# Optimization experiments

Measured on AMD Instinct MI355X. Metric: run time of the kernel, lower is better.

The kernel has to match this reference:

```python
import jax, jax.numpy as jnp
import numpy as np

N_NODES = 50000
N_EDGES = 800000
N_IN = 96
N_HID = 96
N_CLS = 16
P_DROP = 0.5


def setup_inputs() -> dict:
    key = jax.random.key(0)
    ks = jax.random.split(key, 10)
    return {
        "features": jax.random.normal(ks[0], (N_NODES, N_IN), dtype=jnp.float32),
        "edge_weight": jax.random.uniform(ks[1], (N_EDGES,), dtype=jnp.float32),
        "src": jax.random.randint(ks[2], (N_EDGES,), 0, N_NODES),
        "dst": jax.random.randint(ks[3], (N_EDGES,), 0, N_NODES),
        "W0": jax.random.normal(ks[4], (N_IN, N_HID), dtype=jnp.float32) / np.sqrt(N_IN).astype(np.float32),
        "b0": jnp.zeros((N_HID,), dtype=jnp.float32),
        "W1": jax.random.normal(ks[5], (N_HID, N_HID), dtype=jnp.float32) / np.sqrt(N_HID).astype(np.float32),
        "b1": jnp.zeros((N_HID,), dtype=jnp.float32),
        "W2": jax.random.normal(ks[6], (N_HID, N_CLS), dtype=jnp.float32) / np.sqrt(N_HID).astype(np.float32),
        "b2": jnp.zeros((N_CLS,), dtype=jnp.float32),
    }


def reference(features, edge_weight, src, dst, W0, b0, W1, b1, W2, b2):
    N = features.shape[0]
    # Unweighted node degrees (DGL GraphConv norm='both'), clamped to >= 1.
    ones_e = jnp.ones_like(edge_weight)
    out_deg = jnp.clip(jax.ops.segment_sum(ones_e, src, num_segments=N), 1.0)
    in_deg = jnp.clip(jax.ops.segment_sum(ones_e, dst, num_segments=N), 1.0)
    inv_sqrt_out = out_deg ** -0.5  # [N]
    inv_sqrt_in = in_deg ** -0.5    # [N]

    def graph_conv(h, W, b, act):
        h = h * inv_sqrt_out[:, None]
        m = h[src] * edge_weight[:, None]                   # [E, d] gather + edge scale
        agg = jax.ops.segment_sum(m, dst, num_segments=N)   # [N, d] scatter-add
        out = (agg * inv_sqrt_in[:, None]) @ W + b          # D_in^-1/2, then linear + bias
        return act(out) if act is not None else out

    layers = [(W0, b0, jax.nn.relu), (W1, b1, jax.nn.relu), (W2, b2, None)]
    dkey = jax.random.key(42)
    h = features
    for i, (W, b, act) in enumerate(layers):
        keep = jax.random.bernoulli(jax.random.fold_in(dkey, i), 1.0 - P_DROP, h.shape)
        h = jnp.where(keep, h / (1.0 - P_DROP), 0.0)        # dropout p=0.5
        h = graph_conv(h, W, b, act)
    return jax.nn.log_softmax(h, axis=1)
```

## Files before the change

kernel.cpp:

```cpp
#include <hip/hip_runtime.h>
#include <hip/hip_fp16.h>
#include <stdint.h>

#define NNODES 50000
#define NEDGES 800000
#define NHID 96
#define NCLS 16
#define NB ((NNODES + 255) / 256)

#define NC 200
#define NR 4
#define EPB (NEDGES / NC)
#define RNODES (NNODES / NR)
#define RWORDS8 (RNODES / 4)
#define NWORDS8 (NNODES / 4)
#define NDROP4 ((NNODES * NHID / 4 + 255) / 256)

__host__ __device__ inline void tf2x32(uint32_t k0, uint32_t k1, uint32_t x0, uint32_t x1,
                                       uint32_t& o0, uint32_t& o1) {
  uint32_t k2 = k0 ^ k1 ^ 0x1BD11BDAu;
#define TFROT(v, r) (((v) << (r)) | ((v) >> (32 - (r))))
#define TFR(r) { x0 += x1; x1 = TFROT(x1, r); x1 ^= x0; }
  x0 += k0; x1 += k1;
  TFR(13) TFR(15) TFR(26) TFR(6)
  x0 += k1; x1 += k2 + 1u;
  TFR(17) TFR(29) TFR(16) TFR(24)
  x0 += k2; x1 += k0 + 2u;
  TFR(13) TFR(15) TFR(26) TFR(6)
  x0 += k0; x1 += k1 + 3u;
  TFR(17) TFR(29) TFR(16) TFR(24)
  x0 += k1; x1 += k2 + 4u;
  TFR(13) TFR(15) TFR(26) TFR(6)
  x0 += k2; x1 += k0 + 5u;
  o0 = x0; o1 = x1;
#undef TFR
#undef TFROT
}

__device__ inline bool keep_bit(uint32_t k0, uint32_t k1, uint32_t j) {
  uint32_t o0, o1;
  tf2x32(k0, k1, 0u, j, o0, o1);
  return (((o0 ^ o1) >> 31) == 0u);
}

__global__ __launch_bounds__(256) void hist_kernel(
    const int* __restrict__ src, const int* __restrict__ dst,
    uint32_t* __restrict__ slabD, uint32_t* __restrict__ slabS) {
  __shared__ uint32_t HD[RWORDS8];
  __shared__ uint32_t HS[RWORDS8];
  const int tid = threadIdx.x, b = blockIdx.x;
  const int c = b / NR, r = b - c * NR;
  const int e0 = c * EPB, e1 = e0 + EPB;
  const int nbase = r * RNODES;
  for (int w = tid; w < RWORDS8; w += 256) { HD[w] = 0; HS[w] = 0; }
  __syncthreads();
  int e = e0 + tid;
  for (; e + 768 < e1; e += 1024) {
    int d0 = dst[e] - nbase,       d1 = dst[e + 256] - nbase;
    int d2 = dst[e + 512] - nbase, d3 = dst[e + 768] - nbase;
    int s0 = src[e] - nbase,       s1 = src[e + 256] - nbase;
    int s2 = src[e + 512] - nbase, s3 = src[e + 768] - nbase;
    if ((unsigned)d0 < (unsigned)RNODES) atomicAdd(&HD[d0 >> 2], 1u << ((d0 & 3) * 8));
    if ((unsigned)d1 < (unsigned)RNODES) atomicAdd(&HD[d1 >> 2], 1u << ((d1 & 3) * 8));
    if ((unsigned)d2 < (unsigned)RNODES) atomicAdd(&HD[d2 >> 2], 1u << ((d2 & 3) * 8));
    if ((unsigned)d3 < (unsigned)RNODES) atomicAdd(&HD[d3 >> 2], 1u << ((d3 & 3) * 8));
    if ((unsigned)s0 < (unsigned)RNODES) atomicAdd(&HS[s0 >> 2], 1u << ((s0 & 3) * 8));
    if ((unsigned)s1 < (unsigned)RNODES) atomicAdd(&HS[s1 >> 2], 1u << ((s1 & 3) * 8));
    if ((unsigned)s2 < (unsigned)RNODES) atomicAdd(&HS[s2 >> 2], 1u << ((s2 & 3) * 8));
    if ((unsigned)s3 < (unsigned)RNODES) atomicAdd(&HS[s3 >> 2], 1u << ((s3 & 3) * 8));
  }
  for (; e < e1; e += 256) {
    int d = dst[e] - nbase;
    if ((unsigned)d < (unsigned)RNODES) atomicAdd(&HD[d >> 2], 1u << ((d & 3) * 8));
    int s = src[e] - nbase;
    if ((unsigned)s < (unsigned)RNODES) atomicAdd(&HS[s >> 2], 1u << ((s & 3) * 8));
  }
  __syncthreads();
  uint32_t* dpD = slabD + (size_t)b * RWORDS8;
  uint32_t* dpS = slabS + (size_t)b * RWORDS8;
  for (int w = tid; w < RWORDS8; w += 256) { dpD[w] = HD[w]; dpS[w] = HS[w]; }
}

__global__ __launch_bounds__(256) void reduce_base_kernel(
    const uint32_t* __restrict__ slabD, const uint32_t* __restrict__ slabS,
    int* __restrict__ ideg, float* __restrict__ inv_o, float* __restrict__ inv_i,
    uint32_t* __restrict__ rel8) {
  int gw = blockIdx.x * 256 + threadIdx.x;
  if (gw >= NWORDS8) return;
  int r = gw / RWORDS8, lw = gw - r * RWORDS8;
  int n0 = r * RNODES + 4 * lw;
  uint32_t runD = 0, runS = 0;
#pragma unroll 4
  for (int c = 0; c < NC; ++c) {
    rel8[(size_t)c * NWORDS8 + gw] = runD;
    runD += slabD[(size_t)(c * NR + r) * RWORDS8 + lw];
    runS += slabS[(size_t)(c * NR + r) * RWORDS8 + lw];
  }
  int d0 = runD & 0xFF, d1 = (runD >> 8) & 0xFF, d2 = (runD >> 16) & 0xFF, d3 = runD >> 24;
  int o0 = runS & 0xFF, o1 = (runS >> 8) & 0xFF, o2 = (runS >> 16) & 0xFF, o3 = runS >> 24;
  *(int4*)(ideg + n0) = make_int4(d0, d1, d2, d3);
  *(float4*)(inv_i + n0) = make_float4(
      rsqrtf(fmaxf((float)d0, 1.0f)), rsqrtf(fmaxf((float)d1, 1.0f)),
      rsqrtf(fmaxf((float)d2, 1.0f)), rsqrtf(fmaxf((float)d3, 1.0f)));
  *(float4*)(inv_o + n0) = make_float4(
      rsqrtf(fmaxf((float)o0, 1.0f)), rsqrtf(fmaxf((float)o1, 1.0f)),
      rsqrtf(fmaxf((float)o2, 1.0f)), rsqrtf(fmaxf((float)o3, 1.0f)));
}

__global__ __launch_bounds__(256) void scan_blocks_kernel(
    const int* __restrict__ ideg, int* __restrict__ bsum) {
  __shared__ int lds[256];
  const int tid = threadIdx.x;
  int i = blockIdx.x * 256 + tid;
  lds[tid] = (i < NNODES) ? ideg[i] : 0;
  __syncthreads();
  for (int off = 128; off > 0; off >>= 1) {
    if (tid < off) lds[tid] += lds[tid + off];
    __syncthreads();
  }
  if (tid == 0) bsum[blockIdx.x] = lds[0];
}

__global__ __launch_bounds__(256) void scan_top_kernel(
    const int* __restrict__ bsum, int* __restrict__ boff) {
  __shared__ int lds[256];
  const int tid = threadIdx.x;
  int v = (tid < NB) ? bsum[tid] : 0;
  lds[tid] = v;
  __syncthreads();
  for (int off = 1; off < 256; off <<= 1) {
    int t = (tid >= off) ? lds[tid - off] : 0;
    __syncthreads();
    lds[tid] += t;
    __syncthreads();
  }
  if (tid < NB) boff[tid] = lds[tid] - v;
}

__global__ __launch_bounds__(256) void scan_write_kernel(
    const int* __restrict__ ideg, const int* __restrict__ boff,
    int* __restrict__ row_ptr) {
  __shared__ int lds[256];
  const int tid = threadIdx.x;
  int i = blockIdx.x * 256 + tid;
  int v = (i < NNODES) ? ideg[i] : 0;
  lds[tid] = v;
  __syncthreads();
  for (int off = 1; off < 256; off <<= 1) {
    int t = (tid >= off) ? lds[tid - off] : 0;
    __syncthreads();
    lds[tid] += t;
    __syncthreads();
  }
  if (i < NNODES) row_ptr[i] = boff[blockIdx.x] + lds[tid] - v;
  if (i == 0) row_ptr[NNODES] = NEDGES;
}

__global__ __launch_bounds__(256) void fill_drop_kernel(
    const int* __restrict__ src, const int* __restrict__ dst, const float* __restrict__ ew,
    const uint32_t* __restrict__ rel8, const int* __restrict__ row_ptr,
    uint32_t* __restrict__ csr,
    const float* __restrict__ h, const float* __restrict__ inv_o,
    float* __restrict__ X, uint32_t k0, uint32_t k1) {
  __shared__ uint32_t H[RWORDS8];
  const int tid = threadIdx.x, b = blockIdx.x;
  if (b >= NC * NR) {
    int j = ((b - NC * NR) * 256 + tid) * 4;
    if (j < NNODES * NHID) {
      int n = j / NHID;
      float4 hv = *(const float4*)(h + j);
      float sc = 2.0f * inv_o[n];
      float4 o;
      o.x = keep_bit(k0, k1, (uint32_t)(j + 0)) ? hv.x * sc : 0.0f;
      o.y = keep_bit(k0, k1, (uint32_t)(j + 1)) ? hv.y * sc : 0.0f;
      o.z = keep_bit(k0, k1, (uint32_t)(j + 2)) ? hv.z * sc : 0.0f;
      o.w = keep_bit(k0, k1, (uint32_t)(j + 3)) ? hv.w * sc : 0.0f;
      *(float4*)(X + j) = o;
    }
    return;
  }
  const int c = b / NR, r = b - c * NR;
  const int e0 = c * EPB, e1 = e0 + EPB;
  const int nbase = r * RNODES;
  const uint32_t* rel = rel8 + (size_t)c * NWORDS8;
  for (int w = tid; w < RWORDS8; w += 256) H[w] = 0;
  __syncthreads();
  int e = e0 + tid;
  for (; e + 256 < e1; e += 512) {
    int da = dst[e], db = dst[e + 256];
    int sa = src[e], sb = src[e + 256];
    float wa = ew[e], wb = ew[e + 256];
    int la = da - nbase, lb = db - nbase;
    bool ia = (unsigned)la < (unsigned)RNODES;
    bool ib = (unsigned)lb < (unsigned)RNODES;
    if (ia) {
      int sh = (la & 3) * 8;
      uint32_t old = atomicAdd(&H[la >> 2], 1u << sh);
      int rank = (int)((old >> sh) & 0xFFu);
      int rel_v = (int)((rel[da >> 2] >> ((da & 3) * 8)) & 0xFFu);
      int pos = row_ptr[da] + rel_v + rank;
      if ((unsigned)pos < (unsigned)NEDGES) {
        uint32_t v = ((uint32_t)sa << 16) | (uint32_t)__half_as_ushort(__float2half_rn(wa));
        __builtin_nontemporal_store(v, &csr[pos]);
      }
    }
    if (ib) {
      int sh = (lb & 3) * 8;
      uint32_t old = atomicAdd(&H[lb >> 2], 1u << sh);
      int rank = (int)((old >> sh) & 0xFFu);
      int rel_v = (int)((rel[db >> 2] >> ((db & 3) * 8)) & 0xFFu);
      int pos = row_ptr[db] + rel_v + rank;
      if ((unsigned)pos < (unsigned)NEDGES) {
        uint32_t v = ((uint32_t)sb << 16) | (uint32_t)__half_as_ushort(__float2half_rn(wb));
        __builtin_nontemporal_store(v, &csr[pos]);
      }
    }
  }
  for (; e < e1; e += 256) {
    int d = dst[e];
    int ld = d - nbase;
    if ((unsigned)ld < (unsigned)RNODES) {
      int sh = (ld & 3) * 8;
      uint32_t old = atomicAdd(&H[ld >> 2], 1u << sh);
      int rank = (int)((old >> sh) & 0xFFu);
      int rel_v = (int)((rel[d >> 2] >> ((d & 3) * 8)) & 0xFFu);
      int pos = row_ptr[d] + rel_v + rank;
      if ((unsigned)pos < (unsigned)NEDGES) {
        uint32_t v = ((uint32_t)src[e] << 16) | (uint32_t)__half_as_ushort(__float2half_rn(ew[e]));
        __builtin_nontemporal_store(v, &csr[pos]);
      }
    }
  }
}

__global__ __launch_bounds__(256) void gemm96_kernel(
    const float* __restrict__ X, const float* __restrict__ W, __half* __restrict__ Yh) {
  __shared__ float Wl[96 * 96];
  const int tid = threadIdx.x;
  {
    const float4* Wg = (const float4*)W;
    float4* Ws = (float4*)Wl;
#pragma unroll
    for (int i = 0; i < 9; ++i)
      Ws[tid + i * 256] = Wg[tid + i * 256];
  }
  __syncthreads();

  const int cg = tid & 7;
  const int rq = tid >> 3;
  const int row0 = blockIdx.x * 128 + rq * 4;
  const int c0 = cg * 12;

  float acc[4][12];
#pragma unroll
  for (int r = 0; r < 4; ++r)
#pragma unroll
    for (int c = 0; c < 12; ++c) acc[r][c] = 0.f;

  const float* xr[4];
#pragma unroll
  for (int r = 0; r < 4; ++r) {
    int rr = row0 + r; if (rr > NNODES - 1) rr = NNODES - 1;
    xr[r] = X + (size_t)rr * 96;
  }

  for (int k = 0; k < 96; k += 4) {
    float4 x4[4];
#pragma unroll
    for (int r = 0; r < 4; ++r) x4[r] = *(const float4*)(xr[r] + k);
#pragma unroll
    for (int kk = 0; kk < 4; ++kk) {
      const float4* wp = (const float4*)(Wl + (k + kk) * 96 + c0);
      float4 w0 = wp[0], w1 = wp[1], w2 = wp[2];
      float xv[4] = { (&x4[0].x)[kk], (&x4[1].x)[kk], (&x4[2].x)[kk], (&x4[3].x)[kk] };
#pragma unroll
      for (int r = 0; r < 4; ++r) {
        acc[r][0]  += xv[r] * w0.x; acc[r][1]  += xv[r] * w0.y;
        acc[r][2]  += xv[r] * w0.z; acc[r][3]  += xv[r] * w0.w;
        acc[r][4]  += xv[r] * w1.x; acc[r][5]  += xv[r] * w1.y;
        acc[r][6]  += xv[r] * w1.z; acc[r][7]  += xv[r] * w1.w;
        acc[r][8]  += xv[r] * w2.x; acc[r][9]  += xv[r] * w2.y;
        acc[r][10] += xv[r] * w2.z; acc[r][11] += xv[r] * w2.w;
      }
    }
  }

#pragma unroll
  for (int r = 0; r < 4; ++r) {
    int rr = row0 + r;
    if (rr < NNODES) {
      __half2* hp = (__half2*)(Yh + (size_t)rr * 96 + c0);
#pragma unroll
      for (int c = 0; c < 6; ++c)
        hp[c] = __floats2half2_rn(acc[r][2 * c], acc[r][2 * c + 1]);
    }
  }
}

__global__ __launch_bounds__(256) void gemm16_kernel(
    const float* __restrict__ X, const float* __restrict__ W, __half* __restrict__ Y2h) {
  __shared__ float Wl[96 * 16];
  const int tid = threadIdx.x;
  {
    const float4* Wg = (const float4*)W;
    float4* Ws = (float4*)Wl;
    for (int i = tid; i < 384; i += 256) Ws[i] = Wg[i];
  }
  __syncthreads();

  const int row0 = blockIdx.x * 512 + tid * 2;
  const float* xr[2];
#pragma unroll
  for (int r = 0; r < 2; ++r) {
    int rr = row0 + r; if (rr > NNODES - 1) rr = NNODES - 1;
    xr[r] = X + (size_t)rr * 96;
  }

  float acc[2][16];
#pragma unroll
  for (int r = 0; r < 2; ++r)
#pragma unroll
    for (int c = 0; c < 16; ++c) acc[r][c] = 0.f;

  for (int k = 0; k < 96; k += 4) {
    float4 x4[2];
#pragma unroll
    for (int r = 0; r < 2; ++r) x4[r] = *(const float4*)(xr[r] + k);
#pragma unroll
    for (int kk = 0; kk < 4; ++kk) {
      const float4* wp = (const float4*)(Wl + (k + kk) * 16);
      float4 w0 = wp[0], w1 = wp[1], w2 = wp[2], w3 = wp[3];
#pragma unroll
      for (int r = 0; r < 2; ++r) {
        float xv = (&x4[r].x)[kk];
        acc[r][0]  += xv * w0.x; acc[r][1]  += xv * w0.y;
        acc[r][2]  += xv * w0.z; acc[r][3]  += xv * w0.w;
        acc[r][4]  += xv * w1.x; acc[r][5]  += xv * w1.y;
        acc[r][6]  += xv * w1.z; acc[r][7]  += xv * w1.w;
        acc[r][8]  += xv * w2.x; acc[r][9]  += xv * w2.y;
        acc[r][10] += xv * w2.z; acc[r][11] += xv * w2.w;
        acc[r][12] += xv * w3.x; acc[r][13] += xv * w3.y;
        acc[r][14] += xv * w3.z; acc[r][15] += xv * w3.w;
      }
    }
  }

#pragma unroll
  for (int r = 0; r < 2; ++r) {
    int rr = row0 + r;
    if (rr < NNODES) {
      __half2* hp = (__half2*)(Y2h + (size_t)rr * 16);
#pragma unroll
      for (int c = 0; c < 8; ++c)
        hp[c] = __floats2half2_rn(acc[r][2 * c], acc[r][2 * c + 1]);
    }
  }
}

#define ACC16(u0, u1, wt) { \
  float2 g0 = __half22float2(*(__half2*)&u0.x); \
  float2 g1 = __half22float2(*(__half2*)&u0.y); \
  float2 g2 = __half22float2(*(__half2*)&u0.z); \
  float2 g3 = __half22float2(*(__half2*)&u0.w); \
  float2 g4 = __half22float2(*(__half2*)&u1.x); \
  float2 g5 = __half22float2(*(__half2*)&u1.y); \
  float2 g6 = __half22float2(*(__half2*)&u1.z); \
  float2 g7 = __half22float2(*(__half2*)&u1.w); \
  acc[0]  += g0.x * wt; acc[1]  += g0.y * wt; \
  acc[2]  += g1.x * wt; acc[3]  += g1.y * wt; \
  acc[4]  += g2.x * wt; acc[5]  += g2.y * wt; \
  acc[6]  += g3.x * wt; acc[7]  += g3.y * wt; \
  acc[8]  += g4.x * wt; acc[9]  += g4.y * wt; \
  acc[10] += g5.x * wt; acc[11] += g5.y * wt; \
  acc[12] += g6.x * wt; acc[13] += g6.y * wt; \
  acc[14] += g7.x * wt; acc[15] += g7.y * wt; }

__global__ __launch_bounds__(256) void gather96_drop_kernel(
    const __half* __restrict__ Yh, const uint32_t* __restrict__ csr,
    const int* __restrict__ row_ptr, const float* __restrict__ inv_in,
    const float* __restrict__ inv_o, const float* __restrict__ bias,
    float* __restrict__ Xn, uint32_t k0, uint32_t k1) {
  int tid = blockIdx.x * 256 + threadIdx.x;
  int n = tid / 6;
  int q = tid - n * 6;
  if (n >= NNODES) return;
  int beg = row_ptr[n], end = row_ptr[n + 1];
  float acc[16];
#pragma unroll
  for (int i = 0; i < 16; ++i) acc[i] = 0.f;

  int p = beg;
  for (; p + 4 <= end; p += 4) {
    uint32_t pa = csr[p], pb = csr[p + 1], pc = csr[p + 2], pd = csr[p + 3];
    int s0 = pa >> 16, s1 = pb >> 16, s2 = pc >> 16, s3 = pd >> 16;
    if (s0 >= NNODES) s0 = 0;
    if (s1 >= NNODES) s1 = 0;
    if (s2 >= NNODES) s2 = 0;
    if (s3 >= NNODES) s3 = 0;
    float w0 = __half2float(__ushort_as_half((unsigned short)(pa & 0xFFFFu)));
    float w1 = __half2float(__ushort_as_half((unsigned short)(pb & 0xFFFFu)));
    float w2 = __half2float(__ushort_as_half((unsigned short)(pc & 0xFFFFu)));
    float w3 = __half2float(__ushort_as_half((unsigned short)(pd & 0xFFFFu)));
    const uint4* y0 = (const uint4*)(Yh + (size_t)s0 * 96 + q * 16);
    const uint4* y1 = (const uint4*)(Yh + (size_t)s1 * 96 + q * 16);
    const uint4* y2 = (const uint4*)(Yh + (size_t)s2 * 96 + q * 16);
    const uint4* y3 = (const uint4*)(Yh + (size_t)s3 * 96 + q * 16);
    uint4 a0 = y0[0], a1 = y0[1];
    uint4 b0 = y1[0], b1 = y1[1];
    uint4 c0 = y2[0], c1 = y2[1];
    uint4 d0 = y3[0], d1 = y3[1];
    ACC16(a0, a1, w0)
    ACC16(b0, b1, w1)
    ACC16(c0, c1, w2)
    ACC16(d0, d1, w3)
  }
  for (; p + 2 <= end; p += 2) {
    uint32_t pa = csr[p], pb = csr[p + 1];
    int s0 = pa >> 16, s1 = pb >> 16;
    if (s0 >= NNODES) s0 = 0;
    if (s1 >= NNODES) s1 = 0;
    float w0 = __half2float(__ushort_as_half((unsigned short)(pa & 0xFFFFu)));
    float w1 = __half2float(__ushort_as_half((unsigned short)(pb & 0xFFFFu)));
    const uint4* y0 = (const uint4*)(Yh + (size_t)s0 * 96 + q * 16);
    const uint4* y1 = (const uint4*)(Yh + (size_t)s1 * 96 + q * 16);
    uint4 a0 = y0[0], a1 = y0[1];
    uint4 b0 = y1[0], b1 = y1[1];
    ACC16(a0, a1, w0)
    ACC16(b0, b1, w1)
  }
  if (p < end) {
    uint32_t pa = csr[p];
    int s0 = pa >> 16;
    if (s0 >= NNODES) s0 = 0;
    float w0 = __half2float(__ushort_as_half((unsigned short)(pa & 0xFFFFu)));
    const uint4* y0 = (const uint4*)(Yh + (size_t)s0 * 96 + q * 16);
    uint4 a0 = y0[0], a1 = y0[1];
    ACC16(a0, a1, w0)
  }

  float iv = inv_in[n];
  float sc = 2.0f * inv_o[n];
  const float* bp = bias + q * 16;
  float o[16];
#pragma unroll
  for (int i = 0; i < 16; ++i)
    o[i] = fmaxf(acc[i] * iv + bp[i], 0.f) * sc;
  uint32_t jb = (uint32_t)(n * 96 + q * 16);
#pragma unroll
  for (int i = 0; i < 16; ++i)
    o[i] = keep_bit(k0, k1, jb + i) ? o[i] : 0.f;
  float* xp = Xn + (size_t)n * 96 + q * 16;
  *(float4*)(xp + 0)  = make_float4(o[0], o[1], o[2], o[3]);
  *(float4*)(xp + 4)  = make_float4(o[4], o[5], o[6], o[7]);
  *(float4*)(xp + 8)  = make_float4(o[8], o[9], o[10], o[11]);
  *(float4*)(xp + 12) = make_float4(o[12], o[13], o[14], o[15]);
}

__global__ __launch_bounds__(256) void gather16_lsm_kernel(
    const __half* __restrict__ Y2h, const uint32_t* __restrict__ csr,
    const int* __restrict__ row_ptr, const float* __restrict__ inv_in,
    const float* __restrict__ b2, float* __restrict__ out) {
  int n = blockIdx.x * 256 + threadIdx.x;
  if (n >= NNODES) return;
  int beg = row_ptr[n], end = row_ptr[n + 1];
  float acc[16];
#pragma unroll
  for (int i = 0; i < 16; ++i) acc[i] = 0.f;

  int p = beg;
  for (; p + 2 <= end; p += 2) {
    uint32_t pa = csr[p], pb = csr[p + 1];
    int sa = pa >> 16, sb = pb >> 16;
    if (sa >= NNODES) sa = 0;
    if (sb >= NNODES) sb = 0;
    float wa = __half2float(__ushort_as_half((unsigned short)(pa & 0xFFFFu)));
    float wb = __half2float(__ushort_as_half((unsigned short)(pb & 0xFFFFu)));
    const uint4* ya = (const uint4*)(Y2h + (size_t)sa * 16);
    const uint4* yb = (const uint4*)(Y2h + (size_t)sb * 16);
    uint4 a0 = ya[0], a1 = ya[1];
    uint4 b0 = yb[0], b1 = yb[1];
    ACC16(a0, a1, wa)
    ACC16(b0, b1, wb)
  }
  if (p < end) {
    uint32_t pa = csr[p];
    int sa = pa >> 16;
    if (sa >= NNODES) sa = 0;
    float wa = __half2float(__ushort_as_half((unsigned short)(pa & 0xFFFFu)));
    const uint4* ya = (const uint4*)(Y2h + (size_t)sa * 16);
    uint4 a0 = ya[0], a1 = ya[1];
    ACC16(a0, a1, wa)
  }

  float iv = inv_in[n];
  float v[16];
#pragma unroll
  for (int i = 0; i < 16; ++i) v[i] = acc[i] * iv + b2[i];
  float m = v[0];
#pragma unroll
  for (int i = 1; i < 16; i++) m = fmaxf(m, v[i]);
  float s = 0.f;
#pragma unroll
  for (int i = 0; i < 16; i++) s += expf(v[i] - m);
  float ls = logf(s);
  float* orow = out + (size_t)n * 16;
#pragma unroll
  for (int i = 0; i < 16; i++) orow[i] = v[i] - m - ls;
}

extern "C" void kernel_launch(void* const* d_in, const int* in_sizes, int n_in,
                              void* d_out, int out_size, void* d_ws, size_t ws_size,
                              hipStream_t stream) {
  const float* feat = (const float*)d_in[0];
  const float* ew   = (const float*)d_in[1];
  const int*   src  = (const int*)d_in[2];
  const int*   dst  = (const int*)d_in[3];
  const float* W0   = (const float*)d_in[4];
  const float* b0   = (const float*)d_in[5];
  const float* W1   = (const float*)d_in[6];
  const float* b1   = (const float*)d_in[7];
  const float* W2   = (const float*)d_in[8];
  const float* b2   = (const float*)d_in[9];
  float* out = (float*)d_out;

  char* base = (char*)d_ws;
  size_t off = 0;
  auto take = [&](size_t nbytes) {
    void* q = base + off;
    off += (nbytes + 255) & ~(size_t)255;
    return q;
  };
  int*      ideg    = (int*)take((size_t)NNODES * 4);
  int*      row_ptr = (int*)take((size_t)(NNODES + 1) * 4);
  int*      bsum    = (int*)take((size_t)NB * 4);
  int*      boff    = (int*)take((size_t)NB * 4);
  float*    inv_o   = (float*)take((size_t)NNODES * 4);
  float*    inv_i   = (float*)take((size_t)NNODES * 4);
  uint32_t* slabD   = (uint32_t*)take((size_t)NC * NR * RWORDS8 * 4);
  uint32_t* slabS   = (uint32_t*)take((size_t)NC * NR * RWORDS8 * 4);
  uint32_t* rel8    = (uint32_t*)take((size_t)NC * NWORDS8 * 4);
  uint32_t* csr     = (uint32_t*)take((size_t)NEDGES * 4);
  float*    X       = (float*)take((size_t)NNODES * NHID * 4);
  __half*   Yh      = (__half*)take((size_t)NNODES * NHID * 2);
  __half*   Y2h     = (__half*)take((size_t)NNODES * NCLS * 2);
  (void)ws_size; (void)in_sizes; (void)n_in; (void)out_size;

  uint32_t k[3][2];
  for (uint32_t i = 0; i < 3; i++) tf2x32(0u, 42u, 0u, i, k[i][0], k[i][1]);

  const int GW = (NWORDS8 + 255) / 256;

  hist_kernel<<<NC * NR, 256, 0, stream>>>(src, dst, slabD, slabS);
  reduce_base_kernel<<<GW, 256, 0, stream>>>(slabD, slabS, ideg, inv_o, inv_i, rel8);
  scan_blocks_kernel<<<NB, 256, 0, stream>>>(ideg, bsum);
  scan_top_kernel<<<1, 256, 0, stream>>>(bsum, boff);
  scan_write_kernel<<<NB, 256, 0, stream>>>(ideg, boff, row_ptr);
  fill_drop_kernel<<<NC * NR + NDROP4, 256, 0, stream>>>(
      src, dst, ew, rel8, row_ptr, csr, feat, inv_o, X, k[0][0], k[0][1]);

  const int G96  = (NNODES + 127) / 128;
  const int G16  = (NNODES + 511) / 512;
  const int GGD  = (NNODES * 6 + 255) / 256;

  gemm96_kernel<<<G96, 256, 0, stream>>>(X, W0, Yh);
  gather96_drop_kernel<<<GGD, 256, 0, stream>>>(Yh, csr, row_ptr, inv_i, inv_o, b0, X, k[1][0], k[1][1]);
  gemm96_kernel<<<G96, 256, 0, stream>>>(X, W1, Yh);
  gather96_drop_kernel<<<GGD, 256, 0, stream>>>(Yh, csr, row_ptr, inv_i, inv_o, b1, X, k[2][0], k[2][1]);
  gemm16_kernel<<<G16, 256, 0, stream>>>(X, W2, Y2h);
  gather16_lsm_kernel<<<(NNODES + 255) / 256, 256, 0, stream>>>(Y2h, csr, row_ptr, inv_i, b2, out);
}
```

Measured before the change: 292.5 us.

## Fuse degree reduce with decoupled-lookback scan, halve chunk count, widen gather

Merges the reduce, block-scan, top-scan and scan-write kernels into one reduce_scan kernel. It computes row_ptr with a single-pass scan where each block publishes its sum through flags and later blocks spin-wait on earlier ones, removing three launches and the ideg/bsum round trips. The edge chunk count NC drops from 200 to 100, which halves the slab and rel8 traffic but makes each histogram block longer. gather96 now uses 3 threads per node with 32 features each instead of 6 threads with 16, trading more registers and less parallelism for fewer redundant CSR reads. The spin-wait assumes earlier blocks are scheduled first, which holds here with only 49 blocks but is not guaranteed in general.

```diff
diff --git a/kernel.cpp b/kernel.cpp
--- a/kernel.cpp
+++ b/kernel.cpp
@@ -6,14 +6,15 @@
 #define NEDGES 800000
 #define NHID 96
 #define NCLS 16
-#define NB ((NNODES + 255) / 256)
-
-#define NC 200
+
+#define NC 100
 #define NR 4
 #define EPB (NEDGES / NC)
 #define RNODES (NNODES / NR)
 #define RWORDS8 (RNODES / 4)
 #define NWORDS8 (NNODES / 4)
+#define SCANB ((NWORDS8 + 255) / 256)
+#define FILLBLKS (NC * NR)
 #define NDROP4 ((NNODES * NHID / 4 + 255) / 256)
 
 __host__ __device__ inline void tf2x32(uint32_t k0, uint32_t k1, uint32_t x0, uint32_t x1,
@@ -45,10 +46,12 @@
 
 __global__ __launch_bounds__(256) void hist_kernel(
     const int* __restrict__ src, const int* __restrict__ dst,
-    uint32_t* __restrict__ slabD, uint32_t* __restrict__ slabS) {
+    uint32_t* __restrict__ slabD, uint32_t* __restrict__ slabS,
+    uint32_t* __restrict__ flags) {
   __shared__ uint32_t HD[RWORDS8];
   __shared__ uint32_t HS[RWORDS8];
   const int tid = threadIdx.x, b = blockIdx.x;
+  if (b == 0 && tid < SCANB) flags[tid] = 0;
   const int c = b / NR, r = b - c * NR;
   const int e0 = c * EPB, e1 = e0 + EPB;
   const int nbase = r * RNODES;
@@ -81,52 +84,31 @@
   for (int w = tid; w < RWORDS8; w += 256) { dpD[w] = HD[w]; dpS[w] = HS[w]; }
 }
 
-__global__ __launch_bounds__(256) void reduce_base_kernel(
+__global__ __launch_bounds__(256) void reduce_scan_kernel(
     const uint32_t* __restrict__ slabD, const uint32_t* __restrict__ slabS,
-    int* __restrict__ ideg, float* __restrict__ inv_o, float* __restrict__ inv_i,
-    uint32_t* __restrict__ rel8) {
-  int gw = blockIdx.x * 256 + threadIdx.x;
-  if (gw >= NWORDS8) return;
-  int r = gw / RWORDS8, lw = gw - r * RWORDS8;
-  int n0 = r * RNODES + 4 * lw;
+    float* __restrict__ inv_o, float* __restrict__ inv_i,
+    uint32_t* __restrict__ rel8, int* __restrict__ row_ptr,
+    uint32_t* __restrict__ flags) {
+  __shared__ int lds[256];
+  __shared__ int base_s;
+  const int tid = threadIdx.x, b = blockIdx.x;
+  const int gw = b * 256 + tid;
   uint32_t runD = 0, runS = 0;
+  int n0 = 0;
+  if (gw < NWORDS8) {
+    int r = gw / RWORDS8, lw = gw - r * RWORDS8;
+    n0 = r * RNODES + 4 * lw;
 #pragma unroll 4
-  for (int c = 0; c < NC; ++c) {
-    rel8[(size_t)c * NWORDS8 + gw] = runD;
-    runD += slabD[(size_t)(c * NR + r) * RWORDS8 + lw];
-    runS += slabS[(size_t)(c * NR + r) * RWORDS8 + lw];
-  }
-  int d0 = runD & 0xFF, d1 = (runD >> 8) & 0xFF, d2 = (runD >> 16) & 0xFF, d3 = runD >> 24;
-  int o0 = runS & 0xFF, o1 = (runS >> 8) & 0xFF, o2 = (runS >> 16) & 0xFF, o3 = runS >> 24;
-  *(int4*)(ideg + n0) = make_int4(d0, d1, d2, d3);
-  *(float4*)(inv_i + n0) = make_float4(
-      rsqrtf(fmaxf((float)d0, 1.0f)), rsqrtf(fmaxf((float)d1, 1.0f)),
-      rsqrtf(fmaxf((float)d2, 1.0f)), rsqrtf(fmaxf((float)d3, 1.0f)));
-  *(float4*)(inv_o + n0) = make_float4(
-      rsqrtf(fmaxf((float)o0, 1.0f)), rsqrtf(fmaxf((float)o1, 1.0f)),
-      rsqrtf(fmaxf((float)o2, 1.0f)), rsqrtf(fmaxf((float)o3, 1.0f)));
-}
-
-__global__ __launch_bounds__(256) void scan_blocks_kernel(
-    const int* __restrict__ ideg, int* __restrict__ bsum) {
-  __shared__ int lds[256];
-  const int tid = threadIdx.x;
-  int i = blockIdx.x * 256 + tid;
-  lds[tid] = (i < NNODES) ? ideg[i] : 0;
-  __syncthreads();
-  for (int off = 128; off > 0; off >>= 1) {
-    if (tid < off) lds[tid] += lds[tid + off];
-    __syncthreads();
-  }
-  if (tid == 0) bsum[blockIdx.x] = lds[0];
-}
-
-__global__ __launch_bounds__(256) void scan_top_kernel(
-    const int* __restrict__ bsum, int* __restrict__ boff) {
-  __shared__ int lds[256];
-  const int tid = threadIdx.x;
-  int v = (tid < NB) ? bsum[tid] : 0;
-  lds[tid] = v;
+    for (int c = 0; c < NC; ++c) {
+      rel8[(size_t)c * NWORDS8 + gw] = runD;
+      runD += slabD[(size_t)(c * NR + r) * RWORDS8 + lw];
+      runS += slabS[(size_t)(c * NR + r) * RWORDS8 + lw];
+    }
+  }
+  const int d0 = runD & 0xFF, d1 = (runD >> 8) & 0xFF,
+            d2 = (runD >> 16) & 0xFF, d3 = runD >> 24;
+  const int tsum = d0 + d1 + d2 + d3;
+  lds[tid] = tsum;
   __syncthreads();
   for (int off = 1; off < 256; off <<= 1) {
     int t = (tid >= off) ? lds[tid - off] : 0;
@@ -134,26 +116,34 @@
     lds[tid] += t;
     __syncthreads();
   }
-  if (tid < NB) boff[tid] = lds[tid] - v;
-}
-
-__global__ __launch_bounds__(256) void scan_write_kernel(
-    const int* __restrict__ ideg, const int* __restrict__ boff,
-    int* __restrict__ row_ptr) {
-  __shared__ int lds[256];
-  const int tid = threadIdx.x;
-  int i = blockIdx.x * 256 + tid;
-  int v = (i < NNODES) ? ideg[i] : 0;
-  lds[tid] = v;
-  __syncthreads();
-  for (int off = 1; off < 256; off <<= 1) {
-    int t = (tid >= off) ? lds[tid - off] : 0;
-    __syncthreads();
-    lds[tid] += t;
-    __syncthreads();
-  }
-  if (i < NNODES) row_ptr[i] = boff[blockIdx.x] + lds[tid] - v;
-  if (i == 0) row_ptr[NNODES] = NEDGES;
+  const int incl = lds[tid];
+  if (tid == 255) atomicExch(&flags[b], 0x80000000u | (uint32_t)lds[255]);
+  if (tid < 64) {
+    uint32_t part = 0;
+    if (tid < b) {
+      uint32_t v;
+      do { v = atomicAdd(&flags[tid], 0u); } while (!(v & 0x80000000u));
+      part = v & 0x7FFFFFFFu;
+    }
+#pragma unroll
+    for (int off = 32; off > 0; off >>= 1)
+      part += __shfl_down((unsigned)part, off, 64);
+    if (tid == 0) base_s = (int)part;
+  }
+  __syncthreads();
+  const int base = base_s;
+  if (gw < NWORDS8) {
+    int excl = base + incl - tsum;
+    *(int4*)(row_ptr + n0) = make_int4(excl, excl + d0, excl + d0 + d1, excl + d0 + d1 + d2);
+    *(float4*)(inv_i + n0) = make_float4(
+        rsqrtf(fmaxf((float)d0, 1.0f)), rsqrtf(fmaxf((float)d1, 1.0f)),
+        rsqrtf(fmaxf((float)d2, 1.0f)), rsqrtf(fmaxf((float)d3, 1.0f)));
+    int o0 = runS & 0xFF, o1 = (runS >> 8) & 0xFF, o2 = (runS >> 16) & 0xFF, o3 = runS >> 24;
+    *(float4*)(inv_o + n0) = make_float4(
+        rsqrtf(fmaxf((float)o0, 1.0f)), rsqrtf(fmaxf((float)o1, 1.0f)),
+        rsqrtf(fmaxf((float)o2, 1.0f)), rsqrtf(fmaxf((float)o3, 1.0f)));
+    if (gw == NWORDS8 - 1) row_ptr[NNODES] = NEDGES;
+  }
 }
 
 __global__ __launch_bounds__(256) void fill_drop_kernel(
@@ -164,8 +154,8 @@
     float* __restrict__ X, uint32_t k0, uint32_t k1) {
   __shared__ uint32_t H[RWORDS8];
   const int tid = threadIdx.x, b = blockIdx.x;
-  if (b >= NC * NR) {
-    int j = ((b - NC * NR) * 256 + tid) * 4;
+  if (b >= FILLBLKS) {
+    int j = ((b - FILLBLKS) * 256 + tid) * 4;
     if (j < NNODES * NHID) {
       int n = j / NHID;
       float4 hv = *(const float4*)(h + j);
@@ -197,7 +187,7 @@
       int sh = (la & 3) * 8;
       uint32_t old = atomicAdd(&H[la >> 2], 1u << sh);
       int rank = (int)((old >> sh) & 0xFFu);
-      int rel_v = (int)((rel[da >> 2] >> ((da & 3) * 8)) & 0xFFu);
+      int rel_v = (int)((rel[da >> 2] >> sh) & 0xFFu);
       int pos = row_ptr[da] + rel_v + rank;
       if ((unsigned)pos < (unsigned)NEDGES) {
         uint32_t v = ((uint32_t)sa << 16) | (uint32_t)__half_as_ushort(__float2half_rn(wa));
@@ -208,7 +198,7 @@
       int sh = (lb & 3) * 8;
       uint32_t old = atomicAdd(&H[lb >> 2], 1u << sh);
       int rank = (int)((old >> sh) & 0xFFu);
-      int rel_v = (int)((rel[db >> 2] >> ((db & 3) * 8)) & 0xFFu);
+      int rel_v = (int)((rel[db >> 2] >> sh) & 0xFFu);
       int pos = row_ptr[db] + rel_v + rank;
       if ((unsigned)pos < (unsigned)NEDGES) {
         uint32_t v = ((uint32_t)sb << 16) | (uint32_t)__half_as_ushort(__float2half_rn(wb));
@@ -223,7 +213,7 @@
       int sh = (ld & 3) * 8;
       uint32_t old = atomicAdd(&H[ld >> 2], 1u << sh);
       int rank = (int)((old >> sh) & 0xFFu);
-      int rel_v = (int)((rel[d >> 2] >> ((d & 3) * 8)) & 0xFFu);
+      int rel_v = (int)((rel[d >> 2] >> sh) & 0xFFu);
       int pos = row_ptr[d] + rel_v + rank;
       if ((unsigned)pos < (unsigned)NEDGES) {
         uint32_t v = ((uint32_t)src[e] << 16) | (uint32_t)__half_as_ushort(__float2half_rn(ew[e]));
@@ -355,6 +345,72 @@
         hp[c] = __floats2half2_rn(acc[r][2 * c], acc[r][2 * c + 1]);
     }
   }
+}
+
+#define ACCQ(u, B, wt) { \
+  float2 g0 = __half22float2(*(__half2*)&u.x); \
+  float2 g1 = __half22float2(*(__half2*)&u.y); \
+  float2 g2 = __half22float2(*(__half2*)&u.z); \
+  float2 g3 = __half22float2(*(__half2*)&u.w); \
+  acc[B+0] += g0.x * wt; acc[B+1] += g0.y * wt; \
+  acc[B+2] += g1.x * wt; acc[B+3] += g1.y * wt; \
+  acc[B+4] += g2.x * wt; acc[B+5] += g2.y * wt; \
+  acc[B+6] += g3.x * wt; acc[B+7] += g3.y * wt; }
+
+__global__ __launch_bounds__(256) void gather96_drop_kernel(
+    const __half* __restrict__ Yh, const uint32_t* __restrict__ csr,
+    const int* __restrict__ row_ptr, const float* __restrict__ inv_in,
+    const float* __restrict__ inv_o, const float* __restrict__ bias,
+    float* __restrict__ Xn, uint32_t k0, uint32_t k1) {
+  int tid = blockIdx.x * 256 + threadIdx.x;
+  int n = tid / 3;
+  int q = tid - n * 3;
+  if (n >= NNODES) return;
+  int beg = row_ptr[n], end = row_ptr[n + 1];
+  float acc[32];
+#pragma unroll
+  for (int i = 0; i < 32; ++i) acc[i] = 0.f;
+
+  int p = beg;
+  for (; p + 2 <= end; p += 2) {
+    uint32_t pa = csr[p], pb = csr[p + 1];
+    int sa = pa >> 16, sb = pb >> 16;
+    if (sa >= NNODES) sa = 0;
+    if (sb >= NNODES) sb = 0;
+    float wa = __half2float(__ushort_as_half((unsigned short)(pa & 0xFFFFu)));
+    float wb = __half2float(__ushort_as_half((unsigned short)(pb & 0xFFFFu)));
+    const uint4* ya = (const uint4*)(Yh + (size_t)sa * 96 + q * 32);
+    const uint4* yb = (const uint4*)(Yh + (size_t)sb * 96 + q * 32);
+    uint4 a0 = ya[0], a1 = ya[1], a2 = ya[2], a3 = ya[3];
+    uint4 b0 = yb[0], b1 = yb[1], b2 = yb[2], b3 = yb[3];
+    ACCQ(a0, 0, wa) ACCQ(a1, 8, wa) ACCQ(a2, 16, wa) ACCQ(a3, 24, wa)
+    ACCQ(b0, 0, wb) ACCQ(b1, 8, wb) ACCQ(b2, 16, wb) ACCQ(b3, 24, wb)
+  }
+  if (p < end) {
+    uint32_t pa = csr[p];
+    int sa = pa >> 16;
+    if (sa >= NNODES) sa = 0;
+    float wa = __half2float(__ushort_as_half((unsigned short)(pa & 0xFFFFu)));
+    const uint4* ya = (const uint4*)(Yh + (size_t)sa * 96 + q * 32);
+    uint4 a0 = ya[0], a1 = ya[1], a2 = ya[2], a3 = ya[3];
+    ACCQ(a0, 0, wa) ACCQ(a1, 8, wa) ACCQ(a2, 16, wa) ACCQ(a3, 24, wa)
+  }
+
+  float iv = inv_in[n];
+  float sc = 2.0f * inv_o[n];
+  const float* bp = bias + q * 32;
+  float o[32];
+#pragma unroll
+  for (int i = 0; i < 32; ++i)
+    o[i] = fmaxf(acc[i] * iv + bp[i], 0.f) * sc;
+  uint32_t jb = (uint32_t)(n * 96 + q * 32);
+#pragma unroll
+  for (int i = 0; i < 32; ++i)
+    o[i] = keep_bit(k0, k1, jb + i) ? o[i] : 0.f;
+  float* xp = Xn + (size_t)n * 96 + q * 32;
+#pragma unroll
+  for (int i = 0; i < 8; ++i)
+    *(float4*)(xp + 4 * i) = make_float4(o[4 * i], o[4 * i + 1], o[4 * i + 2], o[4 * i + 3]);
 }
 
 #define ACC16(u0, u1, wt) { \
@@ -375,87 +431,6 @@
   acc[12] += g6.x * wt; acc[13] += g6.y * wt; \
   acc[14] += g7.x * wt; acc[15] += g7.y * wt; }
 
-__global__ __launch_bounds__(256) void gather96_drop_kernel(
-    const __half* __restrict__ Yh, const uint32_t* __restrict__ csr,
-    const int* __restrict__ row_ptr, const float* __restrict__ inv_in,
-    const float* __restrict__ inv_o, const float* __restrict__ bias,
-    float* __restrict__ Xn, uint32_t k0, uint32_t k1) {
-  int tid = blockIdx.x * 256 + threadIdx.x;
-  int n = tid / 6;
-  int q = tid - n * 6;
-  if (n >= NNODES) return;
-  int beg = row_ptr[n], end = row_ptr[n + 1];
-  float acc[16];
-#pragma unroll
-  for (int i = 0; i < 16; ++i) acc[i] = 0.f;
-
-  int p = beg;
-  for (; p + 4 <= end; p += 4) {
-    uint32_t pa = csr[p], pb = csr[p + 1], pc = csr[p + 2], pd = csr[p + 3];
-    int s0 = pa >> 16, s1 = pb >> 16, s2 = pc >> 16, s3 = pd >> 16;
-    if (s0 >= NNODES) s0 = 0;
-    if (s1 >= NNODES) s1 = 0;
-    if (s2 >= NNODES) s2 = 0;
-    if (s3 >= NNODES) s3 = 0;
-    float w0 = __half2float(__ushort_as_half((unsigned short)(pa & 0xFFFFu)));
-    float w1 = __half2float(__ushort_as_half((unsigned short)(pb & 0xFFFFu)));
-    float w2 = __half2float(__ushort_as_half((unsigned short)(pc & 0xFFFFu)));
-    float w3 = __half2float(__ushort_as_half((unsigned short)(pd & 0xFFFFu)));
-    const uint4* y0 = (const uint4*)(Yh + (size_t)s0 * 96 + q * 16);
-    const uint4* y1 = (const uint4*)(Yh + (size_t)s1 * 96 + q * 16);
-    const uint4* y2 = (const uint4*)(Yh + (size_t)s2 * 96 + q * 16);
-    const uint4* y3 = (const uint4*)(Yh + (size_t)s3 * 96 + q * 16);
-    uint4 a0 = y0[0], a1 = y0[1];
-    uint4 b0 = y1[0], b1 = y1[1];
-    uint4 c0 = y2[0], c1 = y2[1];
-    uint4 d0 = y3[0], d1 = y3[1];
-    ACC16(a0, a1, w0)
-    ACC16(b0, b1, w1)
-    ACC16(c0, c1, w2)
-    ACC16(d0, d1, w3)
-  }
-  for (; p + 2 <= end; p += 2) {
-    uint32_t pa = csr[p], pb = csr[p + 1];
-    int s0 = pa >> 16, s1 = pb >> 16;
-    if (s0 >= NNODES) s0 = 0;
-    if (s1 >= NNODES) s1 = 0;
-    float w0 = __half2float(__ushort_as_half((unsigned short)(pa & 0xFFFFu)));
-    float w1 = __half2float(__ushort_as_half((unsigned short)(pb & 0xFFFFu)));
-    const uint4* y0 = (const uint4*)(Yh + (size_t)s0 * 96 + q * 16);
-    const uint4* y1 = (const uint4*)(Yh + (size_t)s1 * 96 + q * 16);
-    uint4 a0 = y0[0], a1 = y0[1];
-    uint4 b0 = y1[0], b1 = y1[1];
-    ACC16(a0, a1, w0)
-    ACC16(b0, b1, w1)
-  }
-  if (p < end) {
-    uint32_t pa = csr[p];
-    int s0 = pa >> 16;
-    if (s0 >= NNODES) s0 = 0;
-    float w0 = __half2float(__ushort_as_half((unsigned short)(pa & 0xFFFFu)));
-    const uint4* y0 = (const uint4*)(Yh + (size_t)s0 * 96 + q * 16);
-    uint4 a0 = y0[0], a1 = y0[1];
-    ACC16(a0, a1, w0)
-  }
-
-  float iv = inv_in[n];
-  float sc = 2.0f * inv_o[n];
-  const float* bp = bias + q * 16;
-  float o[16];
-#pragma unroll
-  for (int i = 0; i < 16; ++i)
-    o[i] = fmaxf(acc[i] * iv + bp[i], 0.f) * sc;
-  uint32_t jb = (uint32_t)(n * 96 + q * 16);
-#pragma unroll
-  for (int i = 0; i < 16; ++i)
-    o[i] = keep_bit(k0, k1, jb + i) ? o[i] : 0.f;
-  float* xp = Xn + (size_t)n * 96 + q * 16;
-  *(float4*)(xp + 0)  = make_float4(o[0], o[1], o[2], o[3]);
-  *(float4*)(xp + 4)  = make_float4(o[4], o[5], o[6], o[7]);
-  *(float4*)(xp + 8)  = make_float4(o[8], o[9], o[10], o[11]);
-  *(float4*)(xp + 12) = make_float4(o[12], o[13], o[14], o[15]);
-}
-
 __global__ __launch_bounds__(256) void gather16_lsm_kernel(
     const __half* __restrict__ Y2h, const uint32_t* __restrict__ csr,
     const int* __restrict__ row_ptr, const float* __restrict__ inv_in,
@@ -530,10 +505,8 @@
     off += (nbytes + 255) & ~(size_t)255;
     return q;
   };
-  int*      ideg    = (int*)take((size_t)NNODES * 4);
+  uint32_t* flags   = (uint32_t*)take((size_t)SCANB * 4);
   int*      row_ptr = (int*)take((size_t)(NNODES + 1) * 4);
-  int*      bsum    = (int*)take((size_t)NB * 4);
-  int*      boff    = (int*)take((size_t)NB * 4);
   float*    inv_o   = (float*)take((size_t)NNODES * 4);
   float*    inv_i   = (float*)take((size_t)NNODES * 4);
   uint32_t* slabD   = (uint32_t*)take((size_t)NC * NR * RWORDS8 * 4);
@@ -548,19 +521,14 @@
   uint32_t k[3][2];
   for (uint32_t i = 0; i < 3; i++) tf2x32(0u, 42u, 0u, i, k[i][0], k[i][1]);
 
-  const int GW = (NWORDS8 + 255) / 256;
-
-  hist_kernel<<<NC * NR, 256, 0, stream>>>(src, dst, slabD, slabS);
-  reduce_base_kernel<<<GW, 256, 0, stream>>>(slabD, slabS, ideg, inv_o, inv_i, rel8);
-  scan_blocks_kernel<<<NB, 256, 0, stream>>>(ideg, bsum);
-  scan_top_kernel<<<1, 256, 0, stream>>>(bsum, boff);
-  scan_write_kernel<<<NB, 256, 0, stream>>>(ideg, boff, row_ptr);
-  fill_drop_kernel<<<NC * NR + NDROP4, 256, 0, stream>>>(
+  hist_kernel<<<FILLBLKS, 256, 0, stream>>>(src, dst, slabD, slabS, flags);
+  reduce_scan_kernel<<<SCANB, 256, 0, stream>>>(slabD, slabS, inv_o, inv_i, rel8, row_ptr, flags);
+  fill_drop_kernel<<<FILLBLKS + NDROP4, 256, 0, stream>>>(
       src, dst, ew, rel8, row_ptr, csr, feat, inv_o, X, k[0][0], k[0][1]);
 
   const int G96  = (NNODES + 127) / 128;
   const int G16  = (NNODES + 511) / 512;
-  const int GGD  = (NNODES * 6 + 255) / 256;
+  const int GGD  = (NNODES * 3 + 255) / 256;
 
   gemm96_kernel<<<G96, 256, 0, stream>>>(X, W0, Yh);
   gather96_drop_kernel<<<GGD, 256, 0, stream>>>(Yh, csr, row_ptr, inv_i, inv_o, b0, X, k[1][0], k[1][1]);
```

Result: slower. 301.2 us (+3.0%).
